# Kernel tuning notes

Hardware: AMD Instinct MI355X
Metric: run time of the kernel (lower is better)

The kernel has to match this reference:

```python
import jax, jax.numpy as jnp
import numpy as np

B, S, F = 4, 2048, 1024
D_K = 1024


def setup_inputs() -> dict:
    key = jax.random.key(0)
    ks = jax.random.split(key, 9)
    s_in = 1.0 / np.sqrt(F)
    s_dk = 1.0 / np.sqrt(D_K)
    return {
        "x": jax.random.normal(ks[0], (B, S, F), jnp.float32),
        "Wq": jax.random.normal(ks[1], (F, D_K), jnp.float32) * s_in,
        "bq": jax.random.normal(ks[2], (D_K,), jnp.float32) * s_in,
        "Wk": jax.random.normal(ks[3], (F, D_K), jnp.float32) * s_in,
        "bk": jax.random.normal(ks[4], (D_K,), jnp.float32) * s_in,
        "Wv": jax.random.normal(ks[5], (F, D_K), jnp.float32) * s_in,
        "bv": jax.random.normal(ks[6], (D_K,), jnp.float32) * s_in,
        "Wo": jax.random.normal(ks[7], (D_K, F), jnp.float32) * s_dk,
        "bo": jax.random.normal(ks[8], (F,), jnp.float32) * s_dk,
    }


def reference(x, Wq, bq, Wk, bk, Wv, bv, Wo, bo):
    d_k = Wq.shape[1]
    # init_keys(x): keys/values are projections of the same sequence
    keys = jnp.einsum("bsf,fd->bsd", x, Wk) + bk      # [B,S,d_k]
    values = jnp.einsum("bsf,fd->bsd", x, Wv) + bv    # [B,S,d_k]
    queries = jnp.einsum("bsf,fd->bsd", x, Wq) + bq   # [B,S,d_k]
    # scores[b, q, k] = <queries[b,q], keys[b,k]> / sqrt(d_k)
    scores = jnp.einsum("bqd,bkd->bqk", queries, keys) / jnp.sqrt(
        jnp.asarray(d_k, x.dtype)
    )
    # NOTE: original softmaxes over dim=-2, i.e. over the QUERY axis
    attn = jax.nn.softmax(scores, axis=-2)            # [B,Sq,Sk]
    ctx = jnp.einsum("bqk,bkd->bqd", attn, values)    # [B,S,d_k]
    out = jnp.einsum("bqd,df->bqf", ctx, Wo) + bo     # [B,S,F]
    return out
```

## Files before the change

kernel.cpp:

```cpp
#include <hip/hip_runtime.h>
#include <hip/hip_bf16.h>
#include <cstdint>

typedef __bf16 bf16_t;
typedef __bf16 bf16x8 __attribute__((ext_vector_type(8)));
typedef float  floatx4 __attribute__((ext_vector_type(4)));

typedef const __attribute__((address_space(1))) unsigned int* gptr_t;
typedef __attribute__((address_space(3))) unsigned int* lptr_t;

static __device__ __forceinline__ void gl2lds16(const bf16_t* g, bf16_t* l) {
  __builtin_amdgcn_global_load_lds((gptr_t)g, (lptr_t)l, 16, 0, 0);
}

template<int OUT_BF16, int HAS_BIAS, int EXP_COLSUM, int SPLIT3>
__global__ __launch_bounds__(256, 4)
void gemm_nt(const bf16_t* __restrict__ A, const bf16_t* __restrict__ Bt,
             void* __restrict__ Cv,
             const float* __restrict__ b0, const float* __restrict__ b1,
             const float* __restrict__ b2,
             float* __restrict__ L,
             int M, int N, int K, int ldC, float alpha,
             long sA, long sB, long sC,
             long co0, long co1, long co2,
             int mbShift, int ldTv, long sTv)
{
  __shared__ __align__(16) bf16_t smem[4 * 128 * 32];
  bf16_t* As0 = smem;
  bf16_t* Bs0 = smem + 4096;
  bf16_t* As1 = smem + 8192;
  bf16_t* Bs1 = smem + 12288;

  const int bz = blockIdx.z;
  A  += bz * sA;
  Bt += bz * sB;

  int bx = blockIdx.x, by = blockIdx.y;
  {
    const int gx = gridDim.x, gy = gridDim.y;
    const int nb = gx * gy;
    if (((nb & 7) == 0) && ((gx & 3) == 0) && ((gy & 7) == 0)) {
      const int id   = bx + gx * by;
      const int xcd  = id & 7;
      const int o    = id >> 3;
      const int rows = gy >> 3;
      const int pw   = rows << 2;
      const int p    = o / pw;
      const int r    = o - p * pw;
      by = xcd * rows + (r >> 2);
      bx = (p << 2) + (r & 3);
    }
  }

  const int gn0 = bx * 128;
  const int m0  = by * 128;
  const int tid  = threadIdx.x;
  const int lane = tid & 63;
  const int wave = tid >> 6;
  const int wm   = (wave >> 1) * 64;
  const int wn   = (wave & 1) * 64;
  const int lm   = lane & 15;
  const int quad = lane >> 4;

  int n0 = gn0;
  int which = 0;
  bf16_t* Cb = (bf16_t*)Cv;
  float*  Cf = (float*)Cv;
  const float* bias = b0;
  if (SPLIT3) {
    which = gn0 >> 10;
    n0 = gn0 & 1023;
    Cb += (which == 0) ? co0 : (which == 1) ? co1 : co2;
    bias = (which == 0) ? b0 : (which == 1) ? b1 : b2;
  }

  const int srow   = lane >> 2;
  const int schunk = (lane & 3) * 8;
  const int gchunk = ((lane & 3) ^ ((srow >> 1) & 3)) * 8;
  const int fswz   = ((lm >> 1) & 3) * 8;

  floatx4 acc[4][4];
#pragma unroll
  for (int i = 0; i < 4; ++i)
#pragma unroll
    for (int j = 0; j < 4; ++j)
      acc[i][j] = (floatx4)(0.f);

  for (int kk = 0; kk < K; kk += 64) {
    __syncthreads();
#pragma unroll
    for (int t = 0; t < 2; ++t) {
      const int r = wave * 32 + t * 16 + srow;
      const long ar = (long)(m0  + r) * K + kk + gchunk;
      const long br = (long)(gn0 + r) * K + kk + gchunk;
      gl2lds16(A  + ar,      &As0[r * 32 + schunk]);
      gl2lds16(A  + ar + 32, &As1[r * 32 + schunk]);
      gl2lds16(Bt + br,      &Bs0[r * 32 + schunk]);
      gl2lds16(Bt + br + 32, &Bs1[r * 32 + schunk]);
    }
    __syncthreads();

    {
      bf16x8 af[4], bfr[4];
#pragma unroll
      for (int i = 0; i < 4; ++i)
        af[i] = *(const bf16x8*)&As0[(wm + i * 16 + lm) * 32 + ((quad * 8) ^ fswz)];
#pragma unroll
      for (int j = 0; j < 4; ++j)
        bfr[j] = *(const bf16x8*)&Bs0[(wn + j * 16 + lm) * 32 + ((quad * 8) ^ fswz)];
#pragma unroll
      for (int i = 0; i < 4; ++i)
#pragma unroll
        for (int j = 0; j < 4; ++j)
          acc[i][j] = __builtin_amdgcn_mfma_f32_16x16x32_bf16(af[i], bfr[j],
                                                              acc[i][j], 0, 0, 0);
    }
    {
      bf16x8 af[4], bfr[4];
#pragma unroll
      for (int i = 0; i < 4; ++i)
        af[i] = *(const bf16x8*)&As1[(wm + i * 16 + lm) * 32 + ((quad * 8) ^ fswz)];
#pragma unroll
      for (int j = 0; j < 4; ++j)
        bfr[j] = *(const bf16x8*)&Bs1[(wn + j * 16 + lm) * 32 + ((quad * 8) ^ fswz)];
#pragma unroll
      for (int i = 0; i < 4; ++i)
#pragma unroll
        for (int j = 0; j < 4; ++j)
          acc[i][j] = __builtin_amdgcn_mfma_f32_16x16x32_bf16(af[i], bfr[j],
                                                              acc[i][j], 0, 0, 0);
    }
  }

  if (SPLIT3 && which == 2) {
    __syncthreads();
    bf16_t* myT = smem + wave * (16 * 68);
    const int b  = m0 >> mbShift;
    const int s0 = m0 & ((1 << mbShift) - 1);
    const int r8 = lane >> 3;
    const int c8 = lane & 7;
#pragma unroll
    for (int j = 0; j < 4; ++j) {
      const float bv = HAS_BIAS ? bias[n0 + wn + j * 16 + lm] : 0.f;
#pragma unroll
      for (int i = 0; i < 4; ++i)
#pragma unroll
        for (int r = 0; r < 4; ++r)
          myT[lm * 68 + i * 16 + quad * 4 + r] = (bf16_t)(acc[i][j][r] + bv);
#pragma unroll
      for (int t = 0; t < 2; ++t) {
        const int nr = t * 8 + r8;
        const bf16x8 vv = *(const bf16x8*)&myT[nr * 68 + c8 * 8];
        *(bf16x8*)&Cb[(long)b * sTv + (long)(n0 + wn + j * 16 + nr) * ldTv
                      + s0 + wm + c8 * 8] = vv;
      }
    }
  } else if (OUT_BF16) {
    __syncthreads();
    bf16_t* myEp = smem + wave * (16 * 68);
    const int r8 = lane >> 3;
    const int c8 = lane & 7;
    float cs[4] = {0.f, 0.f, 0.f, 0.f};
#pragma unroll
    for (int i = 0; i < 4; ++i) {
#pragma unroll
      for (int j = 0; j < 4; ++j) {
        const float bv = HAS_BIAS ? bias[n0 + wn + j * 16 + lm] : 0.f;
#pragma unroll
        for (int r = 0; r < 4; ++r) {
          float v = alpha * acc[i][j][r];
          if (EXP_COLSUM) { v = __expf(v); cs[j] += v; }
          v += bv;
          myEp[(quad * 4 + r) * 68 + j * 16 + lm] = (bf16_t)v;
        }
      }
#pragma unroll
      for (int t = 0; t < 2; ++t) {
        const int row = t * 8 + r8;
        const bf16x8 vv = *(const bf16x8*)&myEp[row * 68 + c8 * 8];
        *(bf16x8*)&Cb[bz * sC + (long)(m0 + wm + i * 16 + row) * ldC
                      + n0 + wn + c8 * 8] = vv;
      }
    }
    if (EXP_COLSUM) {
#pragma unroll
      for (int j = 0; j < 4; ++j) {
        float v = cs[j];
        v += __shfl_xor(v, 16);
        v += __shfl_xor(v, 32);
        if (quad == 0)
          atomicAdd(&L[bz * N + gn0 + wn + j * 16 + lm], v);
      }
    }
  } else {
#pragma unroll
    for (int j = 0; j < 4; ++j) {
      const int cn = n0 + wn + j * 16 + lm;
      const float bv = HAS_BIAS ? bias[n0 + wn + j * 16 + lm] : 0.f;
#pragma unroll
      for (int i = 0; i < 4; ++i) {
        const int rbase = m0 + wm + i * 16 + quad * 4;
#pragma unroll
        for (int r = 0; r < 4; ++r)
          Cf[bz * sC + (long)(rbase + r) * ldC + cn] = alpha * acc[i][j][r] + bv;
      }
    }
  }
}

__global__ __launch_bounds__(256)
void prep(const float* __restrict__ x, bf16_t* __restrict__ Xb,
          const float* __restrict__ w0, const float* __restrict__ w1,
          const float* __restrict__ w2, const float* __restrict__ w3,
          bf16_t* __restrict__ outQKV, bf16_t* __restrict__ outO)
{
  __shared__ float tile[32][33];
  const int id = blockIdx.x;
  if (id < 8192) {
    const long i = ((long)id * 256 + threadIdx.x) * 4;
    const float4 v = *(const float4*)(x + i);
    struct alignas(8) B4 { bf16_t a, b, c, d; };
    B4 o; o.a = (bf16_t)v.x; o.b = (bf16_t)v.y; o.c = (bf16_t)v.z; o.d = (bf16_t)v.w;
    *(B4*)(Xb + i) = o;
  } else {
    const int t = id - 8192;
    const int z = t >> 10;
    const int bx = t & 31, by = (t >> 5) & 31;
    const float* in = (z == 0) ? w0 : (z == 1) ? w1 : (z == 2) ? w2 : w3;
    bf16_t* out = (z < 3) ? outQKV + (long)z * 1024 * 1024 : outO;
    const int c0 = bx * 32, r0 = by * 32;
    const int tx = threadIdx.x & 31;
    const int ty = threadIdx.x >> 5;
#pragma unroll
    for (int i = 0; i < 32; i += 8)
      tile[ty + i][tx] = in[(long)(r0 + ty + i) * 1024 + (c0 + tx)];
    __syncthreads();
#pragma unroll
    for (int i = 0; i < 32; i += 8)
      out[(long)(c0 + ty + i) * 1024 + (r0 + tx)] = (bf16_t)tile[tx][ty + i];
  }
}

__global__ __launch_bounds__(256)
void scale_vt(bf16_t* __restrict__ Vt, const float* __restrict__ L, int S)
{
  const long base = ((long)blockIdx.x * blockDim.x + threadIdx.x) * 8;
  const int b  = (int)(base >> 21);
  const int s0 = (int)(base & (long)(S - 1));
  const float* Lb = L + b * S + s0;
  bf16x8 v = *(const bf16x8*)(Vt + base);
#pragma unroll
  for (int j = 0; j < 8; ++j)
    v[j] = (bf16_t)((float)v[j] / Lb[j]);
  *(bf16x8*)(Vt + base) = v;
}

extern "C" void kernel_launch(void* const* d_in, const int* in_sizes, int n_in,
                              void* d_out, int out_size, void* d_ws, size_t ws_size,
                              hipStream_t stream)
{
  const int Bz = 4, S = 2048, F = 1024, DK = 1024;
  const int M = Bz * S;

  const float* x  = (const float*)d_in[0];
  const float* Wq = (const float*)d_in[1];
  const float* bq = (const float*)d_in[2];
  const float* Wk = (const float*)d_in[3];
  const float* bk = (const float*)d_in[4];
  const float* Wv = (const float*)d_in[5];
  const float* bv = (const float*)d_in[6];
  const float* Wo = (const float*)d_in[7];
  const float* bo = (const float*)d_in[8];

  char* ws = (char*)d_ws;
  const size_t MB = 1ull << 20;
  bf16_t* Xb   = (bf16_t*)(ws + 0);
  bf16_t* Sc   = (bf16_t*)(ws + 0);
  bf16_t* Q    = (bf16_t*)(ws + 32 * MB);
  bf16_t* Ctx  = (bf16_t*)(ws + 32 * MB);
  bf16_t* Kb   = (bf16_t*)(ws + 48 * MB);
  bf16_t* Vt   = (bf16_t*)(ws + 64 * MB);
  bf16_t* WcatT= (bf16_t*)(ws + 80 * MB);
  float*  L    = (float*)(ws + 80 * MB);
  bf16_t* WoT  = (bf16_t*)(ws + 86 * MB);

  const long coQ = 16 * MB;
  const long coK = 24 * MB;
  const long coV = 32 * MB;

  prep<<<12288, 256, 0, stream>>>(x, Xb, Wq, Wk, Wv, Wo, WcatT, WoT);

  gemm_nt<1, 1, 0, 1><<<dim3(3 * DK / 128, M / 128, 1), 256, 0, stream>>>(
      Xb, WcatT, (void*)ws, bq, bk, bv, nullptr, M, 3 * DK, F, DK, 1.f,
      0, 0, 0, coQ, coK, coV, 11, S, (long)DK * S);

  hipMemsetAsync(L, 0, (size_t)Bz * S * sizeof(float), stream);
  gemm_nt<1, 0, 1, 0><<<dim3(S / 128, S / 128, Bz), 256, 0, stream>>>(
      Q, Kb, Sc, nullptr, nullptr, nullptr, L, S, S, DK, S, 0.03125f,
      (long)S * DK, (long)S * DK, (long)S * S, 0, 0, 0, 0, 0, 0);

  scale_vt<<<((long)Bz * DK * S / 8) / 256, 256, 0, stream>>>(Vt, L, S);

  gemm_nt<1, 0, 0, 0><<<dim3(DK / 128, S / 128, Bz), 256, 0, stream>>>(
      Sc, Vt, Ctx, nullptr, nullptr, nullptr, nullptr, S, DK, S, DK, 1.f,
      (long)S * S, (long)S * DK, (long)S * DK, 0, 0, 0, 0, 0, 0);

  gemm_nt<0, 1, 0, 0><<<dim3(F / 128, M / 128, 1), 256, 0, stream>>>(
      Ctx, WoT, d_out, bo, nullptr, nullptr, nullptr, M, F, DK, F, 1.f,
      0, 0, 0, 0, 0, 0, 0, 0, 0);
}
```

Measured before the change: 265.3 us.

## Add 256x256-tile 512-thread GEMM for QKV projection and score kernels

Introduces a new gemm256 kernel with 256x256 output tiles, 8 waves, 128KB of double-buffered LDS staged in quarter-steps via global_load_lds, an XCD-aware block remap, and setprio around the MFMA bursts. It replaces the 128x128 GEMM for the fused QKV projection and the exp-colsum score GEMM. The aim is more data reuse per LDS load and better overlap of loads with MFMAs. The cost is much larger LDS and register use per block, so occupancy is lower, and the grid is smaller, which can leave CUs idle.

```diff
diff --git a/kernel.cpp b/kernel.cpp
--- a/kernel.cpp
+++ b/kernel.cpp
@@ -11,6 +11,232 @@
 
 static __device__ __forceinline__ void gl2lds16(const bf16_t* g, bf16_t* l) {
   __builtin_amdgcn_global_load_lds((gptr_t)g, (lptr_t)l, 16, 0, 0);
+}
+
+#define BAR()   asm volatile("s_barrier" ::: "memory")
+#define WLGKM() asm volatile("s_waitcnt lgkmcnt(0)" ::: "memory")
+
+template<int HAS_BIAS, int EXP_COLSUM, int SPLIT3>
+__global__ __launch_bounds__(512, 2)
+void gemm256(const bf16_t* __restrict__ A, const bf16_t* __restrict__ Bt,
+             void* __restrict__ Cv,
+             const float* __restrict__ b0, const float* __restrict__ b1,
+             const float* __restrict__ b2,
+             float* __restrict__ L,
+             int M, int N, int K, int ldC, float alpha,
+             long sA, long sB, long sC,
+             long co0, long co1, long co2,
+             int mbShift, int ldTv, long sTv)
+{
+  __shared__ __align__(16) char smemc[131072];
+
+  const int bz = blockIdx.z;
+  A  += bz * sA;
+  Bt += bz * sB;
+
+  int bx, by;
+  {
+    const int gx = gridDim.x, gy = gridDim.y;
+    const int nwg = gx * gy;
+    int id = blockIdx.x + gx * blockIdx.y;
+    const int q = nwg >> 3, r = nwg & 7;
+    const int xcd = id & 7, o = id >> 3;
+    id = (xcd < r ? xcd * (q + 1) : r * (q + 1) + (xcd - r) * q) + o;
+    bx = id % gx;
+    by = id / gx;
+  }
+
+  const int gn0 = bx * 256;
+  const int m0  = by * 256;
+  const int tid  = threadIdx.x;
+  const int lane = tid & 63;
+  const int wave = tid >> 6;
+  const int wm   = wave >> 2;
+  const int wn   = wave & 3;
+  const int lm   = lane & 15;
+  const int quad = lane >> 4;
+
+  int n0 = gn0, which = 0;
+  bf16_t* Cb = (bf16_t*)Cv;
+  const float* bias = b0;
+  if (SPLIT3) {
+    which = gn0 >> 10;
+    n0 = gn0 & 1023;
+    Cb += (which == 0) ? co0 : (which == 1) ? co1 : co2;
+    bias = (which == 0) ? b0 : (which == 1) ? b1 : b2;
+  }
+
+  const int srow = tid >> 2;
+  const int scol = ((tid ^ (tid >> 3)) & 3) * 8;
+  const bf16_t* pA = A  + (long)(m0  + srow) * K + scol;
+  const bf16_t* pB = Bt + (long)(gn0 + srow) * K + scol;
+
+  const int nt = K >> 6;
+
+  auto STAGE = [&](int s) {
+    if (s >= 4 * nt) return;
+    const int ts  = s >> 2;
+    const int h   = s & 3;
+    const int isA = h & 1;
+    const int kh  = h >> 1;
+    const bf16_t* gp = (isA ? pA : pB) + ts * 64 + kh * 32;
+    char* lp = smemc + (ts & 1) * 65536 + (isA ? 0 : 32768) + kh * 16384
+             + tid * 16;
+    gl2lds16(gp,                (bf16_t*)lp);
+    gl2lds16(gp + (long)128 * K, (bf16_t*)(lp + 8192));
+  };
+
+  const int csz  = ((quad ^ (lm >> 1)) & 3) * 16;
+  const int aoff = (wm * 128 + lm) * 64 + csz;
+  const int boff = (wn * 64  + lm) * 64 + csz;
+  auto LDA = [&](int buf, int ks, int f) {
+    return *(const bf16x8*)(smemc + buf * 65536 + ks * 16384 + aoff + f * 1024);
+  };
+  auto LDB = [&](int buf, int ks, int j) {
+    return *(const bf16x8*)(smemc + buf * 65536 + 32768 + ks * 16384 + boff
+                            + j * 1024);
+  };
+
+  floatx4 acc[8][4];
+#pragma unroll
+  for (int f = 0; f < 8; ++f)
+#pragma unroll
+    for (int j = 0; j < 4; ++j)
+      acc[f][j] = (floatx4)(0.f);
+
+#pragma unroll
+  for (int s = 0; s < 7; ++s) STAGE(s);
+  asm volatile("s_waitcnt vmcnt(6)" ::: "memory");
+  BAR();
+
+  for (int t = 0; t < nt; ++t) {
+    const int buf = t & 1;
+    bf16x8 a[4], b0r[4], b1r[4];
+
+#pragma unroll
+    for (int j = 0; j < 4; ++j) b0r[j] = LDB(buf, 0, j);
+#pragma unroll
+    for (int f = 0; f < 4; ++f) a[f] = LDA(buf, 0, f);
+    STAGE(4 * t + 7);
+    BAR(); WLGKM();
+    __builtin_amdgcn_s_setprio(1);
+#pragma unroll
+    for (int f = 0; f < 4; ++f)
+#pragma unroll
+      for (int j = 0; j < 4; ++j)
+        acc[f][j] = __builtin_amdgcn_mfma_f32_16x16x32_bf16(a[f], b0r[j],
+                                                            acc[f][j], 0, 0, 0);
+    __builtin_amdgcn_s_setprio(0);
+    BAR();
+
+#pragma unroll
+    for (int j = 0; j < 4; ++j) b1r[j] = LDB(buf, 1, j);
+#pragma unroll
+    for (int f = 0; f < 4; ++f) a[f] = LDA(buf, 0, 4 + f);
+    STAGE(4 * t + 8);
+    BAR(); WLGKM();
+    __builtin_amdgcn_s_setprio(1);
+#pragma unroll
+    for (int f = 0; f < 4; ++f)
+#pragma unroll
+      for (int j = 0; j < 4; ++j)
+        acc[4 + f][j] = __builtin_amdgcn_mfma_f32_16x16x32_bf16(a[f], b0r[j],
+                                                                acc[4 + f][j], 0, 0, 0);
+    __builtin_amdgcn_s_setprio(0);
+    BAR();
+
+#pragma unroll
+    for (int f = 0; f < 4; ++f) a[f] = LDA(buf, 1, f);
+    STAGE(4 * t + 9);
+    BAR(); WLGKM();
+    __builtin_amdgcn_s_setprio(1);
+#pragma unroll
+    for (int f = 0; f < 4; ++f)
+#pragma unroll
+      for (int j = 0; j < 4; ++j)
+        acc[f][j] = __builtin_amdgcn_mfma_f32_16x16x32_bf16(a[f], b1r[j],
+                                                            acc[f][j], 0, 0, 0);
+    __builtin_amdgcn_s_setprio(0);
+    BAR();
+
+#pragma unroll
+    for (int f = 0; f < 4; ++f) a[f] = LDA(buf, 1, 4 + f);
+    STAGE(4 * t + 10);
+    BAR(); WLGKM();
+    __builtin_amdgcn_s_setprio(1);
+#pragma unroll
+    for (int f = 0; f < 4; ++f)
+#pragma unroll
+      for (int j = 0; j < 4; ++j)
+        acc[4 + f][j] = __builtin_amdgcn_mfma_f32_16x16x32_bf16(a[f], b1r[j],
+                                                                acc[4 + f][j], 0, 0, 0);
+    __builtin_amdgcn_s_setprio(0);
+    if (t < nt - 2) { asm volatile("s_waitcnt vmcnt(6)" ::: "memory"); }
+    else            { asm volatile("s_waitcnt vmcnt(0)" ::: "memory"); }
+    BAR();
+  }
+
+  const int r8 = lane >> 3;
+  const int c8 = lane & 7;
+
+  if (SPLIT3 && which == 2) {
+    bf16_t* myT = (bf16_t*)(smemc + wave * 4608);
+    const int b  = m0 >> mbShift;
+    const int s0 = m0 & ((1 << mbShift) - 1);
+#pragma unroll
+    for (int j = 0; j < 4; ++j) {
+      const float bv = HAS_BIAS ? bias[n0 + wn * 64 + j * 16 + lm] : 0.f;
+#pragma unroll
+      for (int f = 0; f < 8; ++f)
+#pragma unroll
+        for (int r = 0; r < 4; ++r)
+          myT[lm * 144 + f * 16 + quad * 4 + r] = (bf16_t)(acc[f][j][r] + bv);
+#pragma unroll
+      for (int t2 = 0; t2 < 4; ++t2) {
+        const int dr = (t2 & 1) * 8 + r8;
+        const int ck = (t2 >> 1) * 8 + c8;
+        const bf16x8 vv = *(const bf16x8*)&myT[dr * 144 + ck * 8];
+        *(bf16x8*)&Cb[(long)b * sTv + (long)(n0 + wn * 64 + j * 16 + dr) * ldTv
+                      + s0 + wm * 128 + ck * 8] = vv;
+      }
+    }
+  } else {
+    bf16_t* myEp = (bf16_t*)(smemc + wave * 2176);
+    float csum[4] = {0.f, 0.f, 0.f, 0.f};
+    float bv[4];
+#pragma unroll
+    for (int j = 0; j < 4; ++j)
+      bv[j] = HAS_BIAS ? bias[n0 + wn * 64 + j * 16 + lm] : 0.f;
+#pragma unroll
+    for (int f = 0; f < 8; ++f) {
+#pragma unroll
+      for (int j = 0; j < 4; ++j)
+#pragma unroll
+        for (int r = 0; r < 4; ++r) {
+          float v = acc[f][j][r];
+          if (EXP_COLSUM) { v = __expf(alpha * v); csum[j] += v; }
+          v += bv[j];
+          myEp[(quad * 4 + r) * 68 + j * 16 + lm] = (bf16_t)v;
+        }
+#pragma unroll
+      for (int t2 = 0; t2 < 2; ++t2) {
+        const int row = t2 * 8 + r8;
+        const bf16x8 vv = *(const bf16x8*)&myEp[row * 68 + c8 * 8];
+        *(bf16x8*)&Cb[bz * sC + (long)(m0 + wm * 128 + f * 16 + row) * ldC
+                      + n0 + wn * 64 + c8 * 8] = vv;
+      }
+    }
+    if (EXP_COLSUM) {
+#pragma unroll
+      for (int j = 0; j < 4; ++j) {
+        float v = csum[j];
+        v += __shfl_xor(v, 16);
+        v += __shfl_xor(v, 32);
+        if (quad == 0)
+          atomicAdd(&L[bz * N + gn0 + wn * 64 + j * 16 + lm], v);
+      }
+    }
+  }
 }
 
 template<int OUT_BF16, int HAS_BIAS, int EXP_COLSUM, int SPLIT3>
@@ -290,12 +516,12 @@
 
   prep<<<12288, 256, 0, stream>>>(x, Xb, Wq, Wk, Wv, Wo, WcatT, WoT);
 
-  gemm_nt<1, 1, 0, 1><<<dim3(3 * DK / 128, M / 128, 1), 256, 0, stream>>>(
+  gemm256<1, 0, 1><<<dim3(3 * DK / 256, M / 256, 1), 512, 0, stream>>>(
       Xb, WcatT, (void*)ws, bq, bk, bv, nullptr, M, 3 * DK, F, DK, 1.f,
       0, 0, 0, coQ, coK, coV, 11, S, (long)DK * S);
 
   hipMemsetAsync(L, 0, (size_t)Bz * S * sizeof(float), stream);
-  gemm_nt<1, 0, 1, 0><<<dim3(S / 128, S / 128, Bz), 256, 0, stream>>>(
+  gemm256<0, 1, 0><<<dim3(S / 256, S / 256, Bz), 512, 0, stream>>>(
       Q, Kb, Sc, nullptr, nullptr, nullptr, L, S, S, DK, S, 0.03125f,
       (long)S * DK, (long)S * DK, (long)S * S, 0, 0, 0, 0, 0, 0);
 
```

Measured after the change: 286.1 us. 1.08x slower.
